# Kernel tuning notes

Hardware: AMD Instinct MI355X
Metric: run time of the kernel (lower is better)

## Reference

```python
import jax, jax.numpy as jnp
import numpy as np

B, S, H, NH, HD = 8, 1024, 1024, 16, 64
VALID = 512  # valid tokens per sequence (ragged: each seq half-full)
T = B * VALID  # total_nnz
ROPE_THETA = 10000.0
NEG_INF = -1e9


def rotate_half(x):
    x1, x2 = jnp.split(x, 2, axis=-1)
    return jnp.concatenate((-x2, x1), axis=-1)


def setup_inputs() -> dict:
    key = jax.random.key(0)
    k_h, k_qw, k_ow = jax.random.split(key, 3)
    hidden_states = jax.random.normal(k_h, (T, H), jnp.float32)
    # RoPE cos/sin tables at the positions of the unpadded tokens
    inv_freq = 1.0 / (ROPE_THETA ** (np.arange(0, HD, 2, dtype=np.float32) / HD))  # (HD/2,)
    pos = np.tile(np.arange(VALID, dtype=np.float32), B)  # (T,)
    freqs = pos[:, None] * inv_freq[None, :]  # (T, HD/2)
    emb = np.concatenate([freqs, freqs], axis=-1)  # (T, HD)
    cos = jnp.asarray(np.cos(emb))[:, None, :]  # (T, 1, HD) broadcast over heads
    sin = jnp.asarray(np.sin(emb))[:, None, :]
    # indices of valid tokens in the flattened (B*S) padded layout
    indices = jnp.asarray((np.arange(B)[:, None] * S + np.arange(VALID)[None, :]).reshape(-1).astype(np.int64))
    # additive attention bias: 0 for valid keys, -1e9 for padding keys, shape (B,1,1,S)
    key_valid = np.zeros((B, S), dtype=bool)
    key_valid[:, :VALID] = True
    attention_bias = jnp.where(jnp.asarray(key_valid)[:, None, None, :], 0.0, NEG_INF).astype(jnp.float32)
    qkv_w = jax.random.normal(k_qw, (H, 3 * H), jnp.float32) * 0.02
    qkv_b = jnp.zeros((3 * H,), jnp.float32)
    o_w = jax.random.normal(k_ow, (H, H), jnp.float32) * 0.02
    o_b = jnp.zeros((H,), jnp.float32)
    return {"hidden_states": hidden_states, "cos": cos, "sin": sin,
            "attention_bias": attention_bias, "qkv_w": qkv_w, "qkv_b": qkv_b,
            "o_w": o_w, "o_b": o_b, "indices": indices, "batch": B, "seqlen": S}


def reference(hidden_states, cos, sin, attention_bias, qkv_w, qkv_b, o_w, o_b, indices, batch, seqlen):
    # packed QKV projection on unpadded tokens: (T, 3H)
    qkv = hidden_states @ qkv_w + qkv_b
    q, k, v = jnp.split(qkv, 3, axis=-1)
    q = q.reshape(-1, NH, HD)
    k = k.reshape(-1, NH, HD)
    v = v.reshape(-1, NH, HD)
    # rotary position embedding (applied to unpadded q/k)
    q = q * cos + rotate_half(q) * sin
    k = k * cos + rotate_half(k) * sin

    def pad(x):  # (T, NH, HD) -> (B, S, NH, HD), scatter into zero-padded layout
        return jnp.zeros((batch * seqlen, NH, HD), x.dtype).at[indices].set(x).reshape(batch, seqlen, NH, HD)

    qh = pad(q).transpose(0, 2, 1, 3)  # (B, NH, S, HD)
    kh = pad(k).transpose(0, 2, 1, 3)
    vh = pad(v).transpose(0, 2, 1, 3)
    # scaled dot-product attention with additive bias
    scores = jnp.einsum('bhqd,bhkd->bhqk', qh, kh) / jnp.sqrt(jnp.array(HD, qh.dtype)) + attention_bias
    probs = jax.nn.softmax(scores, axis=-1)
    ctx = jnp.einsum('bhqk,bhkd->bhqd', probs, vh)  # (B, NH, S, HD)
    # unpad and merge heads: gather valid rows from flattened (B*S, H)
    out = ctx.transpose(0, 2, 1, 3).reshape(batch * seqlen, NH * HD)[indices]
    return out @ o_w + o_b  # (T, H)
```

## Files before the change

### kernel.cpp

```cpp
#include <hip/hip_runtime.h>

#define T_TOK 4096
#define HDIM  1024
#define NHEAD 16
#define HEADD 64
#define BATCH 8
#define NVALID 512
#define H3    3072

typedef __bf16 bf16;
typedef __attribute__((ext_vector_type(8))) __bf16 bf16x8;
typedef __attribute__((ext_vector_type(4))) __bf16 bf16x4;
typedef __attribute__((ext_vector_type(4))) float f32x4;

__device__ __forceinline__ void load_lds16(const void* g, void* l) {
  __builtin_amdgcn_global_load_lds(
      (const __attribute__((address_space(1))) unsigned int*)g,
      (__attribute__((address_space(3))) unsigned int*)l, 16, 0, 0);
}

__global__ __launch_bounds__(256) void k_cvt(const float* __restrict__ in,
                                             bf16* __restrict__ out) {
  int i = (blockIdx.x * 256 + threadIdx.x) * 4;
  float4 v = *(const float4*)(in + i);
  bf16x4 o;
  o[0] = (bf16)v.x; o[1] = (bf16)v.y; o[2] = (bf16)v.z; o[3] = (bf16)v.w;
  *(bf16x4*)(out + i) = o;
}

__global__ __launch_bounds__(256) void k_tcvt(const float* __restrict__ W,
                                              bf16* __restrict__ Wt,
                                              int K, int N) {
  __shared__ float t[32][33];
  const int ct = blockIdx.x, rt = blockIdx.y;
  const int c = threadIdx.x & 31, r0 = threadIdx.x >> 5;
#pragma unroll
  for (int kk = 0; kk < 4; ++kk) {
    int r = r0 + kk * 8;
    t[r][c] = W[(size_t)(rt * 32 + r) * N + ct * 32 + c];
  }
  __syncthreads();
#pragma unroll
  for (int kk = 0; kk < 4; ++kk) {
    int n = r0 + kk * 8;
    Wt[(size_t)(ct * 32 + n) * K + rt * 32 + c] = (bf16)t[c][n];
  }
}

template <typename OutT>
__global__ __launch_bounds__(256) void k_gemm(const bf16* __restrict__ A,
                                              const bf16* __restrict__ Bt,
                                              const float* __restrict__ bias,
                                              OutT* __restrict__ C,
                                              int M, int N, int K) {
  __shared__ bf16 As[128 * 32];
  __shared__ bf16 Bs[128 * 32];
  const int tid = threadIdx.x;
  const int lane = tid & 63;
  const int wave = tid >> 6;
  const int wr = wave >> 1, wc = wave & 1;
  const int l15 = lane & 15, g = lane >> 4;
  const int row0 = blockIdx.x * 128, col0 = blockIdx.y * 128;

  f32x4 acc[4][4] = {};

  const bf16* Ag = A + (size_t)(row0 + (tid >> 2)) * K + (tid & 3) * 8;
  const bf16* Bg = Bt + (size_t)(col0 + (tid >> 2)) * K + (tid & 3) * 8;
  const int ldsoff = wave * 64 * 8;

  for (int k0 = 0; k0 < K; k0 += 32) {
    __syncthreads();
    load_lds16(Ag + k0, As + ldsoff);
    load_lds16(Ag + k0 + (size_t)64 * K, As + 2048 + ldsoff);
    load_lds16(Bg + k0, Bs + ldsoff);
    load_lds16(Bg + k0 + (size_t)64 * K, Bs + 2048 + ldsoff);
    __syncthreads();

    bf16x8 af[4], bfr[4];
#pragma unroll
    for (int i = 0; i < 4; ++i)
      af[i] = *(const bf16x8*)(As + (wr * 64 + i * 16 + l15) * 32 + g * 8);
#pragma unroll
    for (int j = 0; j < 4; ++j)
      bfr[j] = *(const bf16x8*)(Bs + (wc * 64 + j * 16 + l15) * 32 + g * 8);
#pragma unroll
    for (int i = 0; i < 4; ++i)
#pragma unroll
      for (int j = 0; j < 4; ++j)
        acc[i][j] = __builtin_amdgcn_mfma_f32_16x16x32_bf16(af[i], bfr[j],
                                                            acc[i][j], 0, 0, 0);
  }

#pragma unroll
  for (int i = 0; i < 4; ++i) {
#pragma unroll
    for (int j = 0; j < 4; ++j) {
      int gc = col0 + wc * 64 + j * 16 + l15;
      float bv = bias ? bias[gc] : 0.f;
#pragma unroll
      for (int e = 0; e < 4; ++e) {
        int gr = row0 + wr * 64 + i * 16 + g * 4 + e;
        C[(size_t)gr * N + gc] = (OutT)(acc[i][j][e] + bv);
      }
    }
  }
}

__global__ __launch_bounds__(256) void k_gemm2k(const bf16* __restrict__ A,
                                                const bf16* __restrict__ Bt,
                                                float* __restrict__ Cp,
                                                int M, int N, int K) {
  __shared__ bf16 As[128 * 32];
  __shared__ bf16 Bs[128 * 32];
  const int tid = threadIdx.x;
  const int lane = tid & 63;
  const int wave = tid >> 6;
  const int wr = wave >> 1, wc = wave & 1;
  const int l15 = lane & 15, g = lane >> 4;
  const int row0 = blockIdx.x * 128, col0 = blockIdx.y * 128;
  const int kbase = blockIdx.z * 512;
  float* C = Cp + (size_t)blockIdx.z * M * N;

  f32x4 acc[4][4] = {};

  const bf16* Ag = A + (size_t)(row0 + (tid >> 2)) * K + kbase + (tid & 3) * 8;
  const bf16* Bg = Bt + (size_t)(col0 + (tid >> 2)) * K + kbase + (tid & 3) * 8;
  const int ldsoff = wave * 64 * 8;

  for (int k0 = 0; k0 < 512; k0 += 32) {
    __syncthreads();
    load_lds16(Ag + k0, As + ldsoff);
    load_lds16(Ag + k0 + (size_t)64 * K, As + 2048 + ldsoff);
    load_lds16(Bg + k0, Bs + ldsoff);
    load_lds16(Bg + k0 + (size_t)64 * K, Bs + 2048 + ldsoff);
    __syncthreads();

    bf16x8 af[4], bfr[4];
#pragma unroll
    for (int i = 0; i < 4; ++i)
      af[i] = *(const bf16x8*)(As + (wr * 64 + i * 16 + l15) * 32 + g * 8);
#pragma unroll
    for (int j = 0; j < 4; ++j)
      bfr[j] = *(const bf16x8*)(Bs + (wc * 64 + j * 16 + l15) * 32 + g * 8);
#pragma unroll
    for (int i = 0; i < 4; ++i)
#pragma unroll
      for (int j = 0; j < 4; ++j)
        acc[i][j] = __builtin_amdgcn_mfma_f32_16x16x32_bf16(af[i], bfr[j],
                                                            acc[i][j], 0, 0, 0);
  }

#pragma unroll
  for (int i = 0; i < 4; ++i)
#pragma unroll
    for (int j = 0; j < 4; ++j) {
      int gc = col0 + wc * 64 + j * 16 + l15;
#pragma unroll
      for (int e = 0; e < 4; ++e) {
        int gr = row0 + wr * 64 + i * 16 + g * 4 + e;
        C[(size_t)gr * N + gc] = acc[i][j][e];
      }
    }
}

__global__ __launch_bounds__(256) void k_red(const float* __restrict__ p0,
                                             const float* __restrict__ p1,
                                             const float* __restrict__ bias,
                                             float* __restrict__ out) {
  int i4 = blockIdx.x * 256 + threadIdx.x;
  float4 a = *(const float4*)(p0 + (size_t)i4 * 4);
  float4 b = *(const float4*)(p1 + (size_t)i4 * 4);
  float4 bv = *(const float4*)(bias + ((i4 * 4) & (HDIM - 1)));
  float4 o;
  o.x = a.x + b.x + bv.x; o.y = a.y + b.y + bv.y;
  o.z = a.z + b.z + bv.z; o.w = a.w + b.w + bv.w;
  *(float4*)(out + (size_t)i4 * 4) = o;
}

__global__ __launch_bounds__(256) void k_rope(const bf16* __restrict__ qkv,
                                              const float* __restrict__ cosT,
                                              const float* __restrict__ sinT,
                                              bf16* __restrict__ Qr,
                                              bf16* __restrict__ Kr,
                                              bf16* __restrict__ Vt) {
  __shared__ bf16 vt[64][72];
  const int blk = blockIdx.x;
  const int tt = blk & 7, h = (blk >> 3) & 15, b = blk >> 7;
  const int tid = threadIdx.x;
  const int r = tid >> 2, q4 = tid & 3;
  const int d0 = q4 * 8;
  const int t = b * NVALID + tt * 64 + r;
  const size_t qrow = (size_t)t * H3;

  bf16x8 qlo = *(const bf16x8*)(qkv + qrow + h * 64 + d0);
  bf16x8 qhi = *(const bf16x8*)(qkv + qrow + h * 64 + d0 + 32);
  bf16x8 klo = *(const bf16x8*)(qkv + qrow + 1024 + h * 64 + d0);
  bf16x8 khi = *(const bf16x8*)(qkv + qrow + 1024 + h * 64 + d0 + 32);
  bf16x8 vlo = *(const bf16x8*)(qkv + qrow + 2048 + h * 64 + d0);
  bf16x8 vhi = *(const bf16x8*)(qkv + qrow + 2048 + h * 64 + d0 + 32);

  const float* cp = cosT + (size_t)t * 64 + d0;
  const float* sp = sinT + (size_t)t * 64 + d0;
  float clo[8], chi[8], slo[8], shi[8];
  {
    float4 a0 = *(const float4*)cp,        a1 = *(const float4*)(cp + 4);
    float4 b0 = *(const float4*)(cp + 32), b1 = *(const float4*)(cp + 36);
    float4 e0 = *(const float4*)sp,        e1 = *(const float4*)(sp + 4);
    float4 f0 = *(const float4*)(sp + 32), f1 = *(const float4*)(sp + 36);
    clo[0]=a0.x; clo[1]=a0.y; clo[2]=a0.z; clo[3]=a0.w;
    clo[4]=a1.x; clo[5]=a1.y; clo[6]=a1.z; clo[7]=a1.w;
    chi[0]=b0.x; chi[1]=b0.y; chi[2]=b0.z; chi[3]=b0.w;
    chi[4]=b1.x; chi[5]=b1.y; chi[6]=b1.z; chi[7]=b1.w;
    slo[0]=e0.x; slo[1]=e0.y; slo[2]=e0.z; slo[3]=e0.w;
    slo[4]=e1.x; slo[5]=e1.y; slo[6]=e1.z; slo[7]=e1.w;
    shi[0]=f0.x; shi[1]=f0.y; shi[2]=f0.z; shi[3]=f0.w;
    shi[4]=f1.x; shi[5]=f1.y; shi[6]=f1.z; shi[7]=f1.w;
  }

  bf16x8 qo0, qo1, ko0, ko1;
#pragma unroll
  for (int i = 0; i < 8; ++i) {
    float ql = (float)qlo[i], qh = (float)qhi[i];
    float kl = (float)klo[i], kh = (float)khi[i];
    qo0[i] = (bf16)(ql * clo[i] - qh * slo[i]);
    qo1[i] = (bf16)(qh * chi[i] + ql * shi[i]);
    ko0[i] = (bf16)(kl * clo[i] - kh * slo[i]);
    ko1[i] = (bf16)(kh * chi[i] + kl * shi[i]);
  }
  const size_t orow = ((size_t)(b * NHEAD + h) * NVALID + tt * 64 + r) * HEADD;
  *(bf16x8*)(Qr + orow + d0) = qo0;
  *(bf16x8*)(Qr + orow + d0 + 32) = qo1;
  *(bf16x8*)(Kr + orow + d0) = ko0;
  *(bf16x8*)(Kr + orow + d0 + 32) = ko1;

  *(bf16x8*)(&vt[r][d0]) = vlo;
  *(bf16x8*)(&vt[r][d0 + 32]) = vhi;
  __syncthreads();
  const int d = tid >> 2;
  const size_t vbase =
      ((size_t)(b * NHEAD + h) * HEADD + d) * NVALID + tt * 64 + q4 * 16;
  bf16x8 o0, o1;
#pragma unroll
  for (int kk = 0; kk < 8; ++kk) o0[kk] = vt[q4 * 16 + kk][d];
#pragma unroll
  for (int kk = 0; kk < 8; ++kk) o1[kk] = vt[q4 * 16 + 8 + kk][d];
  *(bf16x8*)(Vt + vbase) = o0;
  *(bf16x8*)(Vt + vbase + 8) = o1;
}

__global__ __launch_bounds__(256) void k_attn(const bf16* __restrict__ Qr,
                                              const bf16* __restrict__ Kr,
                                              const bf16* __restrict__ Vt,
                                              bf16* __restrict__ ctx) {
  __shared__ bf16 Ks[128 * 64];
  __shared__ bf16 Vs[64 * 128];
  __shared__ bf16 Ps[4][16 * 136];

  const int blk = blockIdx.x;
  const int qt = blk & 7, h = (blk >> 3) & 15, b = blk >> 7;
  const int tid = threadIdx.x;
  const int lane = tid & 63;
  const int wave = tid >> 6;
  const int l15 = lane & 15, g = lane >> 4;

  const size_t bh = (size_t)(b * NHEAD + h);
  const bf16* Qg = Qr + (bh * NVALID + qt * 64 + wave * 16) * HEADD;
  const bf16* Kg = Kr + bh * NVALID * HEADD;
  const bf16* Vg = Vt + bh * HEADD * NVALID;

  bf16x8 qf0 = *(const bf16x8*)(Qg + l15 * HEADD + g * 8);
  bf16x8 qf1 = *(const bf16x8*)(Qg + l15 * HEADD + 32 + g * 8);
#pragma unroll
  for (int i = 0; i < 8; ++i) {
    qf0[i] = (bf16)((float)qf0[i] * 0.125f);
    qf1[i] = (bf16)((float)qf1[i] * 0.125f);
  }

  f32x4 acc[4] = {};
  float mrow[4], srow[4];
#pragma unroll
  for (int e = 0; e < 4; ++e) { mrow[e] = -1e30f; srow[e] = 0.f; }

  const int srK = tid >> 3;
  const int sdK = (tid & 7) << 4;
  const int sdV = tid >> 4;
  const int skV = (tid & 15) << 4;

  bf16* pw = &Ps[wave][0];

  auto stageK = [&](int kb) {
#pragma unroll
    for (int p = 0; p < 4; ++p) {
      int row = p * 32 + srK;
      int d2 = sdK ^ ((row & 7) << 4);
      load_lds16(Kg + (size_t)(kb * 128 + row) * HEADD + (d2 >> 1),
                 (char*)Ks + (p * 256 + wave * 64) * 16);
    }
  };
  auto stageV = [&](int kb) {
#pragma unroll
    for (int p = 0; p < 4; ++p) {
      int d = p * 16 + sdV;
      int k2 = skV ^ ((d & 7) << 4);
      load_lds16(Vg + (size_t)d * NVALID + kb * 128 + (k2 >> 1),
                 (char*)Vs + (p * 256 + wave * 64) * 16);
    }
  };

  stageK(0);

  for (int kb = 0; kb < 4; ++kb) {
    asm volatile("s_waitcnt lgkmcnt(0)" ::: "memory");
    __builtin_amdgcn_s_barrier();
    stageV(kb);
    asm volatile("s_waitcnt vmcnt(4)" ::: "memory");
    __builtin_amdgcn_s_barrier();

    f32x4 sc[8];
#pragma unroll
    for (int f = 0; f < 8; ++f) {
      int krow = f * 16 + l15;
      int swz = (krow & 7) << 4;
      const char* kbase = (const char*)Ks + krow * 128;
      bf16x8 kf0 = *(const bf16x8*)(kbase + ((g * 16) ^ swz));
      bf16x8 kf1 = *(const bf16x8*)(kbase + ((g * 16 + 64) ^ swz));
      f32x4 s = {};
      s = __builtin_amdgcn_mfma_f32_16x16x32_bf16(qf0, kf0, s, 0, 0, 0);
      s = __builtin_amdgcn_mfma_f32_16x16x32_bf16(qf1, kf1, s, 0, 0, 0);
      sc[f] = s;
    }

#pragma unroll
    for (int e = 0; e < 4; ++e) {
      float tm = -1e30f;
#pragma unroll
      for (int f = 0; f < 8; ++f) tm = fmaxf(tm, sc[f][e]);
#pragma unroll
      for (int m = 1; m < 16; m <<= 1) tm = fmaxf(tm, __shfl_xor(tm, m, 64));
      float mnew = fmaxf(mrow[e], tm);
      float corr = __expf(mrow[e] - mnew);
      mrow[e] = mnew;
      srow[e] *= corr;
#pragma unroll
      for (int j = 0; j < 4; ++j) acc[j][e] *= corr;
      float rs = 0.f;
#pragma unroll
      for (int f = 0; f < 8; ++f) {
        float p = __expf(sc[f][e] - mnew);
        sc[f][e] = p;
        rs += p;
      }
#pragma unroll
      for (int m = 1; m < 16; m <<= 1) rs += __shfl_xor(rs, m, 64);
      srow[e] += rs;
    }

#pragma unroll
    for (int f = 0; f < 8; ++f)
#pragma unroll
      for (int e = 0; e < 4; ++e)
        pw[(g * 4 + e) * 136 + f * 16 + l15] = (bf16)sc[f][e];

    asm volatile("s_waitcnt vmcnt(0)" ::: "memory");
    __builtin_amdgcn_s_barrier();

    if (kb < 3) stageK(kb + 1);

#pragma unroll
    for (int kt = 0; kt < 4; ++kt) {
      bf16x8 pf = *(const bf16x8*)(pw + l15 * 136 + kt * 32 + g * 8);
#pragma unroll
      for (int j = 0; j < 4; ++j) {
        int d = j * 16 + l15;
        int inner = (kt * 64 + g * 16) ^ ((d & 7) << 4);
        bf16x8 vf = *(const bf16x8*)((const char*)Vs + d * 256 + inner);
        acc[j] = __builtin_amdgcn_mfma_f32_16x16x32_bf16(pf, vf, acc[j], 0, 0, 0);
      }
    }
  }

#pragma unroll
  for (int e = 0; e < 4; ++e) {
    float inv = 1.f / srow[e];
    int row = qt * 64 + wave * 16 + g * 4 + e;
    size_t obase = ((size_t)b * NVALID + row) * HDIM + h * HEADD;
#pragma unroll
    for (int j = 0; j < 4; ++j)
      ctx[obase + j * 16 + l15] = (bf16)(acc[j][e] * inv);
  }
}

extern "C" void kernel_launch(void* const* d_in, const int* in_sizes, int n_in,
                              void* d_out, int out_size, void* d_ws, size_t ws_size,
                              hipStream_t stream) {
  const float* hidden = (const float*)d_in[0];
  const float* cosT   = (const float*)d_in[1];
  const float* sinT   = (const float*)d_in[2];
  const float* qkv_w  = (const float*)d_in[4];
  const float* qkv_b  = (const float*)d_in[5];
  const float* o_w    = (const float*)d_in[6];
  const float* o_b    = (const float*)d_in[7];
  float* out = (float*)d_out;

  char* ws = (char*)d_ws;
  const size_t MB = 1024 * 1024;
  bf16*  hb  = (bf16*)(ws);
  bf16*  w1t = (bf16*)(ws + 8 * MB);
  bf16*  w2t = (bf16*)(ws + 14 * MB);
  bf16*  qkv = (bf16*)(ws + 16 * MB);
  bf16*  Qr  = (bf16*)(ws + 40 * MB);
  bf16*  Kr  = (bf16*)(ws + 48 * MB);
  bf16*  Vtb = (bf16*)(ws + 56 * MB);
  bf16*  ctx = (bf16*)(ws + 16 * MB);
  float* cp0 = (float*)(ws + 80 * MB);

  k_cvt<<<T_TOK * HDIM / 1024, 256, 0, stream>>>(hidden, hb);
  k_tcvt<<<dim3(H3 / 32, HDIM / 32), 256, 0, stream>>>(qkv_w, w1t, HDIM, H3);
  k_tcvt<<<dim3(HDIM / 32, HDIM / 32), 256, 0, stream>>>(o_w, w2t, HDIM, HDIM);
  k_gemm<bf16><<<dim3(T_TOK / 128, H3 / 128), 256, 0, stream>>>(
      hb, w1t, qkv_b, qkv, T_TOK, H3, HDIM);
  k_rope<<<BATCH * NHEAD * 8, 256, 0, stream>>>(qkv, cosT, sinT, Qr, Kr, Vtb);
  k_attn<<<BATCH * NHEAD * 8, 256, 0, stream>>>(Qr, Kr, Vtb, ctx);
  k_gemm2k<<<dim3(T_TOK / 128, HDIM / 128, 2), 256, 0, stream>>>(
      ctx, w2t, cp0, T_TOK, HDIM, HDIM);
  k_red<<<T_TOK * HDIM / 1024, 256, 0, stream>>>(
      cp0, cp0 + (size_t)T_TOK * HDIM, o_b, out);
}
```

Baseline: 203.6 us.

## Process four query tiles per attention block to reuse staged K/V

Each attention block now handles four 64-row query tiles instead of one, so the grid shrinks from 1024 to 256 blocks and each K/V tile staged into LDS is reused four times. K and V for a key block are staged together at the top of each iteration, which removes the old prefetch of the next K tile that overlapped with the PV product. The change cuts global K/V traffic and staging overhead. In exchange it raises register pressure (four accumulator sets and Q fragments per wave), loses the K prefetch overlap, and leaves only 256 blocks for the GPU's CUs.

New measurement: 214.0 us. 5.1% more time.

```diff
diff --git a/kernel.cpp b/kernel.cpp
--- a/kernel.cpp
+++ b/kernel.cpp
@@ -257,29 +257,36 @@
   __shared__ bf16 Ps[4][16 * 136];
 
   const int blk = blockIdx.x;
-  const int qt = blk & 7, h = (blk >> 3) & 15, b = blk >> 7;
+  const int half = blk & 1, h = (blk >> 1) & 15, b = blk >> 5;
   const int tid = threadIdx.x;
   const int lane = tid & 63;
   const int wave = tid >> 6;
   const int l15 = lane & 15, g = lane >> 4;
 
   const size_t bh = (size_t)(b * NHEAD + h);
-  const bf16* Qg = Qr + (bh * NVALID + qt * 64 + wave * 16) * HEADD;
   const bf16* Kg = Kr + bh * NVALID * HEADD;
   const bf16* Vg = Vt + bh * HEADD * NVALID;
 
-  bf16x8 qf0 = *(const bf16x8*)(Qg + l15 * HEADD + g * 8);
-  bf16x8 qf1 = *(const bf16x8*)(Qg + l15 * HEADD + 32 + g * 8);
-#pragma unroll
-  for (int i = 0; i < 8; ++i) {
-    qf0[i] = (bf16)((float)qf0[i] * 0.125f);
-    qf1[i] = (bf16)((float)qf1[i] * 0.125f);
-  }
-
-  f32x4 acc[4] = {};
-  float mrow[4], srow[4];
-#pragma unroll
-  for (int e = 0; e < 4; ++e) { mrow[e] = -1e30f; srow[e] = 0.f; }
+  bf16x8 qf0[4], qf1[4];
+#pragma unroll
+  for (int q = 0; q < 4; ++q) {
+    const bf16* Qg =
+        Qr + (bh * NVALID + (half * 4 + q) * 64 + wave * 16) * HEADD;
+    qf0[q] = *(const bf16x8*)(Qg + l15 * HEADD + g * 8);
+    qf1[q] = *(const bf16x8*)(Qg + l15 * HEADD + 32 + g * 8);
+#pragma unroll
+    for (int i = 0; i < 8; ++i) {
+      qf0[q][i] = (bf16)((float)qf0[q][i] * 0.125f);
+      qf1[q][i] = (bf16)((float)qf1[q][i] * 0.125f);
+    }
+  }
+
+  f32x4 acc[4][4] = {};
+  float mrow[4][4], srow[4][4];
+#pragma unroll
+  for (int q = 0; q < 4; ++q)
+#pragma unroll
+    for (int e = 0; e < 4; ++e) { mrow[q][e] = -1e30f; srow[q][e] = 0.f; }
 
   const int srK = tid >> 3;
   const int sdK = (tid & 7) << 4;
@@ -288,7 +295,9 @@
 
   bf16* pw = &Ps[wave][0];
 
-  auto stageK = [&](int kb) {
+  for (int kb = 0; kb < 4; ++kb) {
+    asm volatile("s_waitcnt lgkmcnt(0)" ::: "memory");
+    __builtin_amdgcn_s_barrier();
 #pragma unroll
     for (int p = 0; p < 4; ++p) {
       int row = p * 32 + srK;
@@ -296,8 +305,6 @@
       load_lds16(Kg + (size_t)(kb * 128 + row) * HEADD + (d2 >> 1),
                  (char*)Ks + (p * 256 + wave * 64) * 16);
     }
-  };
-  auto stageV = [&](int kb) {
 #pragma unroll
     for (int p = 0; p < 4; ++p) {
       int d = p * 16 + sdV;
@@ -305,89 +312,87 @@
       load_lds16(Vg + (size_t)d * NVALID + kb * 128 + (k2 >> 1),
                  (char*)Vs + (p * 256 + wave * 64) * 16);
     }
-  };
-
-  stageK(0);
-
-  for (int kb = 0; kb < 4; ++kb) {
-    asm volatile("s_waitcnt lgkmcnt(0)" ::: "memory");
-    __builtin_amdgcn_s_barrier();
-    stageV(kb);
     asm volatile("s_waitcnt vmcnt(4)" ::: "memory");
     __builtin_amdgcn_s_barrier();
 
-    f32x4 sc[8];
-#pragma unroll
-    for (int f = 0; f < 8; ++f) {
-      int krow = f * 16 + l15;
-      int swz = (krow & 7) << 4;
-      const char* kbase = (const char*)Ks + krow * 128;
-      bf16x8 kf0 = *(const bf16x8*)(kbase + ((g * 16) ^ swz));
-      bf16x8 kf1 = *(const bf16x8*)(kbase + ((g * 16 + 64) ^ swz));
-      f32x4 s = {};
-      s = __builtin_amdgcn_mfma_f32_16x16x32_bf16(qf0, kf0, s, 0, 0, 0);
-      s = __builtin_amdgcn_mfma_f32_16x16x32_bf16(qf1, kf1, s, 0, 0, 0);
-      sc[f] = s;
-    }
-
+    for (int q = 0; q < 4; ++q) {
+      f32x4 sc[8];
+#pragma unroll
+      for (int f = 0; f < 8; ++f) {
+        int krow = f * 16 + l15;
+        int swz = (krow & 7) << 4;
+        const char* kbase = (const char*)Ks + krow * 128;
+        bf16x8 kf0 = *(const bf16x8*)(kbase + ((g * 16) ^ swz));
+        bf16x8 kf1 = *(const bf16x8*)(kbase + ((g * 16 + 64) ^ swz));
+        f32x4 s = {};
+        s = __builtin_amdgcn_mfma_f32_16x16x32_bf16(qf0[q], kf0, s, 0, 0, 0);
+        s = __builtin_amdgcn_mfma_f32_16x16x32_bf16(qf1[q], kf1, s, 0, 0, 0);
+        sc[f] = s;
+      }
+
+#pragma unroll
+      for (int e = 0; e < 4; ++e) {
+        float tm = -1e30f;
+#pragma unroll
+        for (int f = 0; f < 8; ++f) tm = fmaxf(tm, sc[f][e]);
+#pragma unroll
+        for (int m = 1; m < 16; m <<= 1) tm = fmaxf(tm, __shfl_xor(tm, m, 64));
+        float mnew = fmaxf(mrow[q][e], tm);
+        float corr = __expf(mrow[q][e] - mnew);
+        mrow[q][e] = mnew;
+        srow[q][e] *= corr;
+#pragma unroll
+        for (int j = 0; j < 4; ++j) acc[q][j][e] *= corr;
+        float rs = 0.f;
+#pragma unroll
+        for (int f = 0; f < 8; ++f) {
+          float p = __expf(sc[f][e] - mnew);
+          sc[f][e] = p;
+          rs += p;
+        }
+#pragma unroll
+        for (int m = 1; m < 16; m <<= 1) rs += __shfl_xor(rs, m, 64);
+        srow[q][e] += rs;
+      }
+
+      asm volatile("s_waitcnt lgkmcnt(0)" ::: "memory");
+#pragma unroll
+      for (int f = 0; f < 8; ++f)
+#pragma unroll
+        for (int e = 0; e < 4; ++e)
+          pw[(g * 4 + e) * 136 + f * 16 + l15] = (bf16)sc[f][e];
+
+      if (q == 0) {
+        asm volatile("s_waitcnt vmcnt(0)" ::: "memory");
+        __builtin_amdgcn_s_barrier();
+      }
+
+#pragma unroll
+      for (int kt = 0; kt < 4; ++kt) {
+        bf16x8 pf = *(const bf16x8*)(pw + l15 * 136 + kt * 32 + g * 8);
+#pragma unroll
+        for (int j = 0; j < 4; ++j) {
+          int d = j * 16 + l15;
+          int inner = (kt * 64 + g * 16) ^ ((d & 7) << 4);
+          bf16x8 vf = *(const bf16x8*)((const char*)Vs + d * 256 + inner);
+          acc[q][j] = __builtin_amdgcn_mfma_f32_16x16x32_bf16(pf, vf,
+                                                              acc[q][j], 0, 0, 0);
+        }
+      }
+    }
+  }
+
+#pragma unroll
+  for (int q = 0; q < 4; ++q)
 #pragma unroll
     for (int e = 0; e < 4; ++e) {
-      float tm = -1e30f;
-#pragma unroll
-      for (int f = 0; f < 8; ++f) tm = fmaxf(tm, sc[f][e]);
-#pragma unroll
-      for (int m = 1; m < 16; m <<= 1) tm = fmaxf(tm, __shfl_xor(tm, m, 64));
-      float mnew = fmaxf(mrow[e], tm);
-      float corr = __expf(mrow[e] - mnew);
-      mrow[e] = mnew;
-      srow[e] *= corr;
-#pragma unroll
-      for (int j = 0; j < 4; ++j) acc[j][e] *= corr;
-      float rs = 0.f;
-#pragma unroll
-      for (int f = 0; f < 8; ++f) {
-        float p = __expf(sc[f][e] - mnew);
-        sc[f][e] = p;
-        rs += p;
-      }
-#pragma unroll
-      for (int m = 1; m < 16; m <<= 1) rs += __shfl_xor(rs, m, 64);
-      srow[e] += rs;
-    }
-
-#pragma unroll
-    for (int f = 0; f < 8; ++f)
-#pragma unroll
-      for (int e = 0; e < 4; ++e)
-        pw[(g * 4 + e) * 136 + f * 16 + l15] = (bf16)sc[f][e];
-
-    asm volatile("s_waitcnt vmcnt(0)" ::: "memory");
-    __builtin_amdgcn_s_barrier();
-
-    if (kb < 3) stageK(kb + 1);
-
-#pragma unroll
-    for (int kt = 0; kt < 4; ++kt) {
-      bf16x8 pf = *(const bf16x8*)(pw + l15 * 136 + kt * 32 + g * 8);
-#pragma unroll
-      for (int j = 0; j < 4; ++j) {
-        int d = j * 16 + l15;
-        int inner = (kt * 64 + g * 16) ^ ((d & 7) << 4);
-        bf16x8 vf = *(const bf16x8*)((const char*)Vs + d * 256 + inner);
-        acc[j] = __builtin_amdgcn_mfma_f32_16x16x32_bf16(pf, vf, acc[j], 0, 0, 0);
-      }
-    }
-  }
-
-#pragma unroll
-  for (int e = 0; e < 4; ++e) {
-    float inv = 1.f / srow[e];
-    int row = qt * 64 + wave * 16 + g * 4 + e;
-    size_t obase = ((size_t)b * NVALID + row) * HDIM + h * HEADD;
-#pragma unroll
-    for (int j = 0; j < 4; ++j)
-      ctx[obase + j * 16 + l15] = (bf16)(acc[j][e] * inv);
-  }
+      float inv = 1.f / srow[q][e];
+      int row = (half * 4 + q) * 64 + wave * 16 + g * 4 + e;
+      size_t obase = ((size_t)b * NVALID + row) * HDIM + h * HEADD;
+#pragma unroll
+      for (int j = 0; j < 4; ++j)
+        ctx[obase + j * 16 + l15] = (bf16)(acc[q][j][e] * inv);
+    }
 }
 
 extern "C" void kernel_launch(void* const* d_in, const int* in_sizes, int n_in,
@@ -420,7 +425,7 @@
   k_gemm<bf16><<<dim3(T_TOK / 128, H3 / 128), 256, 0, stream>>>(
       hb, w1t, qkv_b, qkv, T_TOK, H3, HDIM);
   k_rope<<<BATCH * NHEAD * 8, 256, 0, stream>>>(qkv, cosT, sinT, Qr, Kr, Vtb);
-  k_attn<<<BATCH * NHEAD * 8, 256, 0, stream>>>(Qr, Kr, Vtb, ctx);
+  k_attn<<<BATCH * NHEAD * 2, 256, 0, stream>>>(Qr, Kr, Vtb, ctx);
   k_gemm2k<<<dim3(T_TOK / 128, HDIM / 128, 2), 256, 0, stream>>>(
       ctx, w2t, cp0, T_TOK, HDIM, HDIM);
   k_red<<<T_TOK * HDIM / 1024, 256, 0, stream>>>(
```
